# Kernel tuning notes

Hardware: AMD Instinct MI355X
Metric: run time of the kernel (lower is better)

Reference implementation:

```python
import jax, jax.numpy as jnp
import numpy as np

T_DAYS, IN_DIM, H = 50000, 12, 512
PIN, POUT, OUT_DIM = 27, 3, 2
# physical_forward scale factors applied to the column means
SCALES = np.array([400,1,1,1,1,12,10,10,1,1,1,1,1,10,1,1,1,5,1,1,4,1,1,180,1,1,10], np.float32)
# last-layer bias of parnet chosen so constrained params land near published PRELES defaults
BIAS27 = np.array([1.03,0.45,0.118,3.0,0.748,1.1,0.05,1.85,-0.18,0.035,-0.2007,0.5,-0.364,
                   0.0324,0.874,0.07,0.8473,0.12,1.2,0.33,1.0,0.0,0.0,1.1,0.0,0.0,2.0], np.float32)

def _elu(v):
    return jnp.where(v > 0, v, jnp.expm1(v))

def _constrain(p):
    # faithful jax port of parameter_constraint (clamp/relu/sigmoid per column)
    sig = jax.nn.sigmoid
    cols = [jnp.clip(p[:,0],0,2), jax.nn.relu(p[:,1]), jax.nn.relu(p[:,2]), p[:,3],
            jnp.clip(p[:,4],0,2.5), jnp.clip(p[:,5],0.01,3), jnp.clip(p[:,6],-0.2,2.1),
            jnp.clip(p[:,7],0.23,3.0), jnp.clip(p[:,8],-1,0), jnp.clip(p[:,9],0,0.7),
            sig(p[:,10]), p[:,11], p[:,12], jnp.clip(p[:,13],0,1.0), jnp.clip(p[:,14],0,1.2),
            jnp.clip(p[:,15],0,2.5), sig(p[:,16]), jnp.clip(p[:,17],0,1), p[:,18],
            jnp.clip(p[:,19],0,1/0.75), jax.nn.relu(p[:,20]), jax.nn.relu(p[:,21]), p[:,22],
            jax.nn.relu(p[:,23]), jax.nn.relu(p[:,24]), jax.nn.relu(p[:,25]), jax.nn.relu(p[:,26])]
    return jnp.stack(cols, axis=1)

def _preles(pm, cin):
    # PRELES daily LUE model (etmodel=0, LOGFLAG=0, t0=-999 so fPheno=1), run as one lax.scan
    (soildepth, ThetaFC, ThetaPWP, tauDrainage, beta, tau, S0, Smax, kappa, gamma,
     soilthres, bCO2, xCO2, ETbeta, ETkappa, ETchi, ETsoilthres, ETnu, MeltCoef,
     I0, CWmax, SnowThreshold, T0, SWinit, CWinit, SOGinit, Sinit) = [pm[i] for i in range(27)]
    fcap = ThetaFC * soildepth

    def step(carry, day):
        S, theta, snow, canw = carry
        precip, tair, par, vpd, fapar, co2 = day[0], day[1], day[2], day[3], day[4], day[6]
        # temperature acclimation state and fS
        S = S + (tair - S) / tau
        fS = jnp.minimum(jnp.maximum(S - S0, 0.0) / Smax, 1.0)
        # GPP modifiers
        thetavol = theta / soildepth
        REW = (thetavol - ThetaPWP) / (ThetaFC - ThetaPWP)
        fD = jnp.minimum(jnp.exp(kappa * vpd), 1.0)
        fW = jnp.where(REW < soilthres, jnp.where(REW > 0.01, REW / soilthres, 0.0), 1.0)
        fL = 1.0 / (gamma * par + 1.0)
        fE = jnp.minimum(fD, fW)
        gpp380 = beta * par * fapar * fS * fL * fE
        gpp = gpp380 * (1.0 + bCO2 * jnp.log(co2 / 380.0))
        # interception + canopy water store
        intercepted = jnp.where(tair > SnowThreshold, precip * I0 * fapar / 0.75, 0.0)
        rain = precip - intercepted
        cap = CWmax * fapar
        over = intercepted + canw > cap
        small_cw = CWmax <= 1e-8
        tf = jnp.where(small_cw, rain + intercepted,
                       jnp.where(over, rain + intercepted + canw - cap, rain))
        canw = jnp.where(small_cw, canw, jnp.where(over, cap, canw + intercepted))
        # snow pack (degree-day melt)
        newsnow = jnp.where(tair < SnowThreshold, tf, 0.0)
        tf = tf - newsnow
        melt = jnp.where(tair >= T0, MeltCoef * (tair - T0), 0.0)
        melt = jnp.minimum(melt, snow + newsnow)
        snow = snow + newsnow - melt
        # evapotranspiration, etmodel = 0
        fWet = jnp.where(REW < ETsoilthres, jnp.where(REW > 0.01, REW / ETsoilthres, 0.0), 1.0)
        fWet = jnp.where(canw > 1e-8, 1.0, fWet)
        fCO2et = 1.0 + xCO2 * jnp.log(co2 / 380.0)
        transp = vpd * ETbeta * gpp380 / jnp.power(vpd, ETkappa) * jnp.power(jnp.maximum(fW, 1e-12), ETnu) * fCO2et
        evap = ETchi * (1.0 - fapar) * fWet * par
        et = transp + evap
        # soil water balance: evaporate wet canopy then snow, rest from soil
        canw2 = jnp.maximum(canw - et, 0.0)
        rem = jnp.maximum(et - canw, 0.0)
        snow2 = jnp.maximum(snow - rem, 0.0)
        etsoil = jnp.maximum(rem - snow, 0.0)
        st0 = jnp.maximum(theta + tf + melt - etsoil, 1e-4)
        drain = jnp.where(tauDrainage > 0, jnp.maximum(st0 - fcap, 0.0) / tauDrainage, 0.0)
        theta = st0 - drain
        return (S, theta, snow2, canw2), (gpp, et, theta)

    init = (Sinit, SWinit, SOGinit, CWinit)
    _, (GPP, ET, SWout) = jax.lax.scan(step, init, cin)
    return GPP, ET, SWout

def setup_inputs():
    key = jax.random.key(0)
    ks = jax.random.split(key, 12)
    x = jax.random.normal(ks[0], (T_DAYS, IN_DIM), jnp.float32)
    u = jax.random.uniform(ks[1], (T_DAYS, 7), jnp.float32)
    tn = jax.random.normal(ks[2], (T_DAYS,), jnp.float32)
    doy = (jnp.arange(T_DAYS) % 365 + 1).astype(jnp.float32)
    seas = jnp.sin(2 * jnp.pi * (doy - 120) / 365.0)
    precip = jnp.where(u[:, 0] > 0.7, u[:, 0] * 20.0, 0.0)        # mm/day
    tair = 5.0 + 12.0 * seas + 3.0 * tn                            # degC
    par = jnp.maximum(10.0 + 8.0 * seas + 3.0 * jax.random.normal(ks[3], (T_DAYS,), jnp.float32), 0.1)
    vpd = 0.1 + 2.0 * u[:, 3]                                      # kPa, kept > 0.1
    fapar = 0.3 + 0.5 * u[:, 4]
    co2 = 380.0 + 40.0 * u[:, 6]                                   # ppm
    cin = jnp.stack([precip, tair, par, vpd, fapar, doy, co2], axis=1)
    def lin(k, fi, fo, scale, bias=None):
        w = jax.random.normal(k, (fi, fo), jnp.float32) * scale
        b = jnp.zeros((fo,), jnp.float32) if bias is None else jnp.asarray(bias)
        return w, b
    pW0, pb0 = lin(ks[4], IN_DIM, H, 1.0 / np.sqrt(IN_DIM))
    pW1, pb1 = lin(ks[5], H, H, 1.0 / np.sqrt(H))
    pW2, pb2 = lin(ks[6], H, PIN, 0.01, BIAS27)
    rW0, rb0 = lin(ks[7], POUT, H, 1.0 / np.sqrt(POUT))
    rW1, rb1 = lin(ks[8], H, H, 1.0 / np.sqrt(H))
    rW2, rb2 = lin(ks[9], H, OUT_DIM, 1.0 / np.sqrt(H))
    sw = jnp.array([150.0, 50.0], jnp.float32)
    return dict(x=x, cin=cin, sw=sw, tp=1,
                pW0=pW0, pb0=pb0, pW1=pW1, pb1=pb1, pW2=pW2, pb2=pb2,
                rW0=rW0, rb0=rb0, rW1=rW1, rb1=rb1, rW2=rW2, rb2=rb2)

def reference(x, cin, sw, tp, pW0, pb0, pW1, pb1, pW2, pb2, rW0, rb0, rW1, rb1, rW2, rb2):
    # parnet: Linear -> ELU -> Linear -> Linear (single ELU due to add_module name reuse)
    h = _elu(x @ pW0 + pb0)
    h = h @ pW1 + pb1
    praw = h @ pW2 + pb2                      # [T, 27]
    p = _constrain(praw)
    pm = p.mean(axis=0) * jnp.asarray(SCALES)  # per-parameter mean, physical scaling
    GPP, ET, SW = _preles(pm, cin)
    ppreds = jnp.stack([GPP, ET, (SW - sw[0]) / sw[1]], axis=1)  # tp is not None path
    # resnet: Linear -> ELU -> Linear -> Linear
    g = _elu(ppreds @ rW0 + rb0)
    g = g @ rW1 + rb1
    y_hat = g @ rW2 + rb2
    return y_hat, ppreds
```

## Files before the change

kernel.cpp:

```cpp
#include <hip/hip_runtime.h>
#include <hip/hip_bf16.h>

#define T_DAYS   50000
#define HDIM     512
#define NP       27
#define NROWBLK  196

#define NCHUNK   1024
#define CHUNK_L  49
#define WARM     512
#define ITERS    (WARM + CHUNK_L)
#define GRP      8
#define NG       72
#define DPAD     50944
#define DBLK     199

static_assert(NG*GRP >= ITERS, "scan must cover all iterations");
static_assert((NG & 1) == 0, "NG must be even for the ping-pong");
static_assert(1023*CHUNK_L + (NG+1)*GRP - 1 < DPAD, "prefetch stays in padded records");

#define OFF_PJ    0
#define OFF_PR0   20480
#define OFF_RW12  22528
#define OFF_B12   23552
#define OFF_RB12  23579
#define OFF_PART  23584
#define OFF_PM    28880
#define OFF_DA    29184
#define OFF_DB    (OFF_DA + DPAD*4)
#define OFF_DC    (OFF_DB + DPAD*4)
#define OFF_PPT   (OFF_DC + DPAD)
#define WS_FAST_FLOATS (OFF_PPT + CHUNK_L*NCHUNK*3)
#define WS_FAST_BYTES  ((size_t)WS_FAST_FLOATS * 4)

typedef float f32x4 __attribute__((ext_vector_type(4)));

__constant__ float c_SCALES[NP] = {400,1,1,1,1,12,10,10,1,1,1,1,1,10,1,1,1,5,1,1,4,1,1,180,1,1,10};

__device__ __forceinline__ float sane(float v, float lo, float hi) {
  v = (v == v) ? v : 0.f;
  return fminf(fmaxf(v, lo), hi);
}

__device__ __forceinline__ void ldg4(f32x4& d, const f32x4* p) {
  asm volatile("global_load_dwordx4 %0, %1, off" : "=v"(d) : "v"(p));
}
__device__ __forceinline__ void ldg1(float& d, const float* p) {
  asm volatile("global_load_dword %0, %1, off" : "=v"(d) : "v"(p));
}
__device__ __forceinline__ void wait_vm0() {
  asm volatile("s_waitcnt vmcnt(0)" ::: "memory");
  __builtin_amdgcn_sched_barrier(0);
}

__global__ void k_prep(const float* pW0, const float* pb0, const float* pW1,
                       const float* pb1, const float* pW2, const float* pb2,
                       const float* rW0, const float* rb0, const float* rW1,
                       const float* rb1, const float* rW2, const float* rb2,
                       float* ws) {
  __shared__ __align__(16) float col[HDIM];
  const int bid = blockIdx.x, tid = threadIdx.x;
  if (bid < NP) {
    for (int k = tid; k < HDIM; k += 256) col[k] = pW2[k*NP + bid];
    __syncthreads();
    const float4* c4 = (const float4*)col;
    for (int i = tid; i < HDIM; i += 256) {
      const float4* wrow = (const float4*)(pW1 + i*HDIM);
      float acc = 0.f;
      #pragma unroll 4
      for (int k = 0; k < HDIM/4; ++k) {
        float4 w = wrow[k], cv = c4[k];
        acc += w.x*cv.x + w.y*cv.y + w.z*cv.z + w.w*cv.w;
      }
      ws[OFF_PJ + i*40 + 12 + bid] = acc;
    }
    if (tid == 0) {
      float acc = 0.f;
      for (int k = 0; k < HDIM; ++k) acc += pb1[k] * col[k];
      ws[OFF_B12 + bid] = acc + pb2[bid];
    }
  } else if (bid < NP + 2) {
    const int j2 = bid - NP;
    for (int k = tid; k < HDIM; k += 256) col[k] = rW2[k*2 + j2];
    __syncthreads();
    const float4* c4 = (const float4*)col;
    for (int i = tid; i < HDIM; i += 256) {
      const float4* wrow = (const float4*)(rW1 + i*HDIM);
      float acc = 0.f;
      #pragma unroll 4
      for (int k = 0; k < HDIM/4; ++k) {
        float4 w = wrow[k], cv = c4[k];
        acc += w.x*cv.x + w.y*cv.y + w.z*cv.z + w.w*cv.w;
      }
      ws[OFF_RW12 + i*2 + j2] = acc;
    }
    if (tid == 0) {
      float acc = 0.f;
      for (int k = 0; k < HDIM; ++k) acc += rb1[k] * col[k];
      ws[OFF_RB12 + j2] = acc + rb2[j2];
    }
  } else {
    for (int j = tid; j < HDIM; j += 256) {
      for (int k = 0; k < 12; ++k) ws[OFF_PJ + j*40 + k] = pW0[k*HDIM + j];
      ws[OFF_PJ + j*40 + 39] = pb0[j];
      float4 v;
      v.x = rW0[0*HDIM + j]; v.y = rW0[1*HDIM + j];
      v.z = rW0[2*HDIM + j]; v.w = rb0[j];
      ((float4*)(ws + OFF_PR0))[j] = v;
    }
  }
}

__global__ void __launch_bounds__(256) k_parnet(const float* x, float* ws) {
  __shared__ float4 spj[256*10];
  const int t = blockIdx.x*256 + threadIdx.x;

  float xr[12];
  if (t < T_DAYS) {
    const float4* xp = (const float4*)(x + t*12);
    float4 x0 = xp[0], x1 = xp[1], x2 = xp[2];
    xr[0]=x0.x; xr[1]=x0.y; xr[2]=x0.z; xr[3]=x0.w;
    xr[4]=x1.x; xr[5]=x1.y; xr[6]=x1.z; xr[7]=x1.w;
    xr[8]=x2.x; xr[9]=x2.y; xr[10]=x2.z; xr[11]=x2.w;
  } else {
    #pragma unroll
    for (int k = 0; k < 12; ++k) xr[k] = 0.f;
  }

  float acc[NP];
  #pragma unroll
  for (int c = 0; c < NP; ++c) acc[c] = ws[OFF_B12 + c];

  for (int half = 0; half < 2; ++half) {
    __syncthreads();
    const float4* src = ((const float4*)(ws + OFF_PJ)) + half*2560;
    for (int idx = threadIdx.x; idx < 2560; idx += 256) spj[idx] = src[idx];
    __syncthreads();
    for (int j = 0; j < 256; ++j) {
      const float4* row = &spj[j*10];
      float4 a = row[0], b = row[1], cc = row[2];
      float wf[28];
      #pragma unroll
      for (int q = 0; q < 7; ++q) {
        float4 v = row[3 + q];
        wf[4*q] = v.x; wf[4*q+1] = v.y; wf[4*q+2] = v.z; wf[4*q+3] = v.w;
      }
      float h = a.x*xr[0] + a.y*xr[1] + a.z*xr[2] + a.w*xr[3]
              + b.x*xr[4] + b.y*xr[5] + b.z*xr[6] + b.w*xr[7]
              + cc.x*xr[8] + cc.y*xr[9] + cc.z*xr[10] + cc.w*xr[11]
              + wf[27];
      h = h > 0.f ? h : (__expf(h) - 1.f);
      #pragma unroll
      for (int c = 0; c < NP; ++c) acc[c] += h * wf[c];
    }
  }

  auto clip = [] (float v, float lo, float hi) { return fminf(fmaxf(v, lo), hi); };
  acc[0]  = clip(acc[0], 0.f, 2.f);
  acc[1]  = fmaxf(acc[1], 0.f);
  acc[2]  = fmaxf(acc[2], 0.f);
  acc[4]  = clip(acc[4], 0.f, 2.5f);
  acc[5]  = clip(acc[5], 0.01f, 3.f);
  acc[6]  = clip(acc[6], -0.2f, 2.1f);
  acc[7]  = clip(acc[7], 0.23f, 3.0f);
  acc[8]  = clip(acc[8], -1.f, 0.f);
  acc[9]  = clip(acc[9], 0.f, 0.7f);
  acc[10] = 1.f/(1.f + __expf(-acc[10]));
  acc[13] = clip(acc[13], 0.f, 1.0f);
  acc[14] = clip(acc[14], 0.f, 1.2f);
  acc[15] = clip(acc[15], 0.f, 2.5f);
  acc[16] = 1.f/(1.f + __expf(-acc[16]));
  acc[17] = clip(acc[17], 0.f, 1.f);
  acc[19] = clip(acc[19], 0.f, (float)(1.0/0.75));
  acc[20] = fmaxf(acc[20], 0.f);
  acc[21] = fmaxf(acc[21], 0.f);
  acc[23] = fmaxf(acc[23], 0.f);
  acc[24] = fmaxf(acc[24], 0.f);
  acc[25] = fmaxf(acc[25], 0.f);
  acc[26] = fmaxf(acc[26], 0.f);
  if (t >= T_DAYS) {
    #pragma unroll
    for (int c = 0; c < NP; ++c) acc[c] = 0.f;
  }

  #pragma unroll
  for (int c = 0; c < NP; ++c) {
    float v = acc[c];
    #pragma unroll
    for (int off = 32; off >= 1; off >>= 1) v += __shfl_down(v, off, 64);
    acc[c] = v;
  }
  __shared__ float red[4][NP];
  const int wv = threadIdx.x >> 6, ln = threadIdx.x & 63;
  if (ln == 0) {
    #pragma unroll
    for (int c = 0; c < NP; ++c) red[wv][c] = acc[c];
  }
  __syncthreads();
  if (threadIdx.x < NP) {
    float s = red[0][threadIdx.x] + red[1][threadIdx.x] + red[2][threadIdx.x] + red[3][threadIdx.x];
    ws[OFF_PART + blockIdx.x*NP + threadIdx.x] = s;
  }
}

__global__ void k_finalize(float* ws) {
  const int c = threadIdx.x;
  if (c < NP) {
    float s = 0.f;
    for (int b = 0; b < NROWBLK; ++b) s += ws[OFF_PART + b*NP + c];
    ws[OFF_PM + c] = sane(s * (1.f/(float)T_DAYS) * c_SCALES[c], -1e6f, 1e6f);
  }
}

__global__ void __launch_bounds__(256) k_days(const float* ws_in, const float* cin, float* ws) {
  const int tp = blockIdx.x*256 + threadIdx.x;
  if (tp >= DPAD) return;
  const float* pm = ws_in + OFF_PM;
  const float beta = pm[4], kappa = pm[8], gamma = pm[9], bCO2 = pm[11], xCO2 = pm[12];
  const float ETbeta = pm[13], ETkappa = pm[14], ETchi = pm[15], MeltCoef = pm[18];
  const float I0 = pm[19], CWmax = pm[20], SnowThr = pm[21], T0 = pm[22];

  int t = tp - WARM;
  t = t < 0 ? 0 : (t >= T_DAYS ? T_DAYS - 1 : t);
  const float precip = sane(cin[t*7+0], 0.f, 1e4f);
  const float tair   = sane(cin[t*7+1], -150.f, 150.f);
  const float par    = sane(cin[t*7+2], 0.f, 1e4f);
  const float vpd    = sane(cin[t*7+3], 1e-3f, 1e3f);
  const float fapar  = sane(cin[t*7+4], 0.f, 1.f);
  const float co2    = sane(cin[t*7+6], 1.f, 1e5f);

  const float logc = __logf(co2 * (1.f/380.f));
  const float fD   = fminf(__expf(kappa*vpd), 1.f);
  const float G    = beta * par * fapar * (1.f/(gamma*par + 1.f));
  const float Cc   = 1.f + bCO2*logc;
  const float Bq   = ETbeta * __powf(vpd, 1.f - ETkappa) * (1.f + xCO2*logc);
  const float E    = ETchi * (1.f - fapar) * par;
  const float icpt = (tair > SnowThr) ? precip*I0*fapar*(1.f/0.75f) : 0.f;
  const float rain = precip - icpt;
  const float cap  = CWmax * fapar;
  const float mpot = (tair >= T0) ? MeltCoef*(tair - T0) : 0.f;

  ((float4*)(ws + OFF_DA))[tp] = make_float4(fD, G*Cc, Bq*G, E);
  ((float4*)(ws + OFF_DB))[tp] = make_float4(rain, cap, icpt, mpot);
  ws[OFF_DC + tp] = tair;
}

__global__ void __launch_bounds__(64, 1) k_scan_fast(float* ws, const float* sw) {
  const int lane = threadIdx.x;
  const int c = blockIdx.x*64 + lane;
  const float* pm = ws + OFF_PM;
  const float soildepth = pm[0], ThetaFC = pm[1], ThetaPWP = pm[2];
  const float tauD = pm[3], tau = pm[5], S0 = pm[6], Smax = pm[7];
  const float soilthres = pm[10], ETsoilthres = pm[16], ETnu = pm[17];
  const float SnowThr = pm[21];
  const float SWinit = pm[23], CWinit = pm[24], SOGinit = pm[25], Sinit = pm[26];
  const float CWmax = pm[20];

  float dFC = ThetaFC - ThetaPWP; if (!(fabsf(dFC) > 1e-12f)) dFC = 1e-12f;
  float sd  = soildepth;          if (!(fabsf(sd)  > 1e-12f)) sd  = 1e-12f;

  const float invtau = 1.f/fmaxf(tau, 1e-6f), invSmax = 1.f/fmaxf(Smax, 1e-12f);
  const float rc1 = 1.f/(sd*dFC);
  const float rc0 = -ThetaPWP/dFC;
  const float inv_st = 1.f/fmaxf(soilthres, 1e-30f);
  const float inv_est = 1.f/fmaxf(ETsoilthres, 1e-30f);
  const float fcap = ThetaFC*soildepth;
  const float invtauD = (tauD > 0.f) ? 1.f/tauD : 0.f;
  const bool small_cw = (CWmax <= 1e-8f);
  const float sw0 = sane(sw[0], -1e6f, 1e6f);
  const float sw1v = sw[1];
  const float invsw1 = 1.f/((fabsf(sw1v) > 1e-12f) ? sw1v : 1e-12f);

  float S = Sinit, theta = SWinit, snow = SOGinit, canw = CWinit;
  const int i_lo = (c*CHUNK_L < WARM) ? (WARM - c*CHUNK_L) : 0;

  const f32x4* gA = ((const f32x4*)(ws + OFF_DA)) + c*CHUNK_L;
  const f32x4* gB = ((const f32x4*)(ws + OFF_DB)) + c*CHUNK_L;
  const float* gC = (ws + OFF_DC) + c*CHUNK_L;
  float* ppt = ws + OFF_PPT;

  auto step = [&](const f32x4 dA, const f32x4 dB, const float tairv, const int i,
                  float& o0, float& o1, float& o2) {
    if (i < i_lo) return;
    const float fD = dA.x, GC = dA.y, BG = dA.z, E = dA.w;
    const float rain = dB.x, cap = dB.y, icpt = dB.z, mpot = dB.w;

    S += (tairv - S)*invtau;
    S = fminf(fmaxf(S, -1e4f), 1e4f);
    const float fS = fminf(fmaxf(S - S0, 0.f)*invSmax, 1.f);

    const float REW = theta*rc1 + rc0;
    float fW   = (REW >= soilthres)   ? 1.f : ((REW > 0.01f) ? REW*inv_st  : 0.f);
    float fWet = (REW >= ETsoilthres) ? 1.f : ((REW > 0.01f) ? REW*inv_est : 0.f);

    const float precip = rain + icpt;
    const bool over = (icpt + canw > cap);
    const float tf  = small_cw ? precip : (over ? precip + canw - cap : rain);
    const float cw  = small_cw ? canw   : (over ? cap : canw + icpt);
    if (cw > 1e-8f) fWet = 1.f;

    const bool cold = (tairv < SnowThr);
    const float newsnow = cold ? tf : 0.f;
    const float tf2     = cold ? 0.f : tf;
    const float sn = snow + newsnow;
    const float snow_mid = fmaxf(sn - mpot, 0.f);
    const float melt = sn - snow_mid;

    const float sfe = fS * fminf(fD, fW);
    float pw = 1.f;
    if (fW < 1.f) pw = __powf(fmaxf(fW, 1e-12f), ETnu);
    const float transp = BG*sfe*pw;
    const float evap = E*fWet;
    const float et = transp + evap;

    canw = fminf(fmaxf(cw - et, 0.f), 1e4f);
    const float rem = fmaxf(et - cw, 0.f);
    snow = fminf(fmaxf(snow_mid - rem, 0.f), 1e6f);
    const float etsoil = fmaxf(rem - snow_mid, 0.f);
    const float st0 = fmaxf(theta + tf2 + melt - etsoil, 1e-4f);
    const float dr = fmaxf(st0 - fcap, 0.f)*invtauD;
    theta = fminf(fmaxf(st0 - dr, 1e-4f), 1e6f);

    o0 = sane(GC*sfe, -1e6f, 1e6f);
    o1 = sane(et, -1e6f, 1e6f);
    o2 = sane((theta - sw0)*invsw1, -1e6f, 1e6f);
  };

  f32x4 A0[GRP], B0[GRP]; float C0[GRP];
  f32x4 A1[GRP], B1[GRP]; float C1[GRP];
  float poA[GRP*3], poB[GRP*3];

#define ISSUE(GG, A, B, C) do { \
  _Pragma("unroll") for (int k = 0; k < GRP; ++k) { \
    const int ii = (GG)*GRP + k; \
    ldg4(A[k], gA + ii); ldg4(B[k], gB + ii); ldg1(C[k], gC + ii); \
  } __builtin_amdgcn_sched_barrier(0); } while (0)

#define COMPUTE(GG, A, B, C, PO) do { \
  _Pragma("unroll") for (int k = 0; k < GRP; ++k) \
    step(A[k], B[k], C[k], (GG)*GRP + k, PO[k*3], PO[k*3+1], PO[k*3+2]); \
  __builtin_amdgcn_sched_barrier(0); } while (0)

#define FLUSH(GF, PO) do { \
  _Pragma("unroll") for (int k = 0; k < GRP; ++k) { \
    const int io = (GF)*GRP + k - WARM; \
    if (io >= 0 && io < CHUNK_L) { \
      float* pp = ppt + (io*NCHUNK + c)*3; \
      pp[0] = PO[k*3]; pp[1] = PO[k*3+1]; pp[2] = PO[k*3+2]; \
    } } } while (0)

  ISSUE(0, A0, B0, C0);
  for (int g = 0; g < NG; g += 2) {
    wait_vm0();
    ISSUE(g + 1, A1, B1, C1);
    if (g > 0) FLUSH(g - 1, poB);
    COMPUTE(g, A0, B0, C0, poA);

    wait_vm0();
    ISSUE(g + 2, A0, B0, C0);
    FLUSH(g, poA);
    COMPUTE(g + 1, A1, B1, C1, poB);
  }
  FLUSH(NG - 1, poB);

#undef ISSUE
#undef COMPUTE
#undef FLUSH
}

__global__ void __launch_bounds__(256) k_resnet_fast(const float* ws, float* out) {
  __shared__ float4 spr[HDIM];
  __shared__ float2 srw[HDIM];
  for (int idx = threadIdx.x; idx < HDIM; idx += 256) {
    spr[idx] = ((const float4*)(ws + OFF_PR0))[idx];
    srw[idx] = ((const float2*)(ws + OFF_RW12))[idx];
  }
  __syncthreads();
  const int t = blockIdx.x*256 + threadIdx.x;
  if (t >= T_DAYS) return;
  const int c = t / CHUNK_L, i = t - c*CHUNK_L;
  const int r = (i*NCHUNK + c)*3;
  const float p0 = ws[OFF_PPT + r + 0];
  const float p1 = ws[OFF_PPT + r + 1];
  const float p2 = ws[OFF_PPT + r + 2];
  float y0 = ws[OFF_RB12], y1 = ws[OFF_RB12 + 1];
  for (int j = 0; j < HDIM; ++j) {
    const float4 a = spr[j];
    float g = p0*a.x + p1*a.y + p2*a.z + a.w;
    g = g > 0.f ? g : (__expf(g) - 1.f);
    const float2 r2 = srw[j];
    y0 += g*r2.x; y1 += g*r2.y;
  }
  out[t*2 + 0] = sane(y0, -1e6f, 1e6f);
  out[t*2 + 1] = sane(y1, -1e6f, 1e6f);
  out[2*T_DAYS + t*3 + 0] = p0;
  out[2*T_DAYS + t*3 + 1] = p1;
  out[2*T_DAYS + t*3 + 2] = p2;
}

struct DayR { float fD, G, Cc, Bq, E, rain, cap, icpt, mpot, tair; };

__device__ __forceinline__ DayR mkday(const float* cin, int t,
    float beta, float kappa, float gamma, float bCO2, float xCO2, float ETbeta,
    float ETkappa, float ETchi, float MeltCoef, float I0, float CWmax,
    float SnowThr, float T0) {
  int tt = t < 0 ? 0 : (t >= T_DAYS ? T_DAYS - 1 : t);
  const float precip = sane(cin[tt*7+0], 0.f, 1e4f);
  const float tair   = sane(cin[tt*7+1], -150.f, 150.f);
  const float par    = sane(cin[tt*7+2], 0.f, 1e4f);
  const float vpd    = sane(cin[tt*7+3], 1e-3f, 1e3f);
  const float fapar  = sane(cin[tt*7+4], 0.f, 1.f);
  const float co2    = sane(cin[tt*7+6], 1.f, 1e5f);
  const float logc = __logf(co2 * (1.f/380.f));
  DayR d;
  d.fD   = fminf(__expf(kappa*vpd), 1.f);
  d.G    = beta * par * fapar * (1.f/(gamma*par + 1.f));
  d.Cc   = 1.f + bCO2*logc;
  d.Bq   = ETbeta * __powf(vpd, 1.f - ETkappa) * (1.f + xCO2*logc);
  d.E    = ETchi * (1.f - fapar) * par;
  d.icpt = (tair > SnowThr) ? precip*I0*fapar*(1.f/0.75f) : 0.f;
  d.rain = precip - d.icpt;
  d.cap  = CWmax * fapar;
  d.mpot = (tair >= T0) ? MeltCoef*(tair - T0) : 0.f;
  d.tair = tair;
  return d;
}

__global__ void __launch_bounds__(64) k_scan_slow(const float* ws, const float* cin,
                                                 const float* sw, float* out) {
  const int c = blockIdx.x*64 + threadIdx.x;
  const float* pm = ws + OFF_PM;
  const float soildepth = pm[0], ThetaFC = pm[1], ThetaPWP = pm[2];
  const float tauD = pm[3], beta = pm[4], tau = pm[5], S0 = pm[6], Smax = pm[7];
  const float kappa = pm[8], gamma = pm[9], soilthres = pm[10], bCO2 = pm[11];
  const float xCO2 = pm[12], ETbeta = pm[13], ETkappa = pm[14], ETchi = pm[15];
  const float ETsoilthres = pm[16], ETnu = pm[17], MeltCoef = pm[18], I0 = pm[19];
  const float CWmax = pm[20], SnowThr = pm[21], T0 = pm[22];
  const float SWinit = pm[23], CWinit = pm[24], SOGinit = pm[25], Sinit = pm[26];

  float dFC = ThetaFC - ThetaPWP; if (!(fabsf(dFC) > 1e-12f)) dFC = 1e-12f;
  float sd  = soildepth;          if (!(fabsf(sd)  > 1e-12f)) sd  = 1e-12f;

  const float invtau = 1.f/fmaxf(tau, 1e-6f), invSmax = 1.f/fmaxf(Smax, 1e-12f);
  const float rc1 = 1.f/(sd*dFC);
  const float rc0 = -ThetaPWP/dFC;
  const float inv_st = 1.f/fmaxf(soilthres, 1e-30f);
  const float inv_est = 1.f/fmaxf(ETsoilthres, 1e-30f);
  const float fcap = ThetaFC*soildepth;
  const float invtauD = (tauD > 0.f) ? 1.f/tauD : 0.f;
  const bool small_cw = (CWmax <= 1e-8f);
  const float sw0 = sane(sw[0], -1e6f, 1e6f);
  const float sw1v = sw[1];
  const float invsw1 = 1.f/((fabsf(sw1v) > 1e-12f) ? sw1v : 1e-12f);

  float S = Sinit, theta = SWinit, snow = SOGinit, canw = CWinit;
  const int s  = c*CHUNK_L - WARM;
  const int e0 = c*CHUNK_L;

  DayR dA = mkday(cin, s,   beta,kappa,gamma,bCO2,xCO2,ETbeta,ETkappa,ETchi,MeltCoef,I0,CWmax,SnowThr,T0);
  DayR dB = mkday(cin, s+1, beta,kappa,gamma,bCO2,xCO2,ETbeta,ETkappa,ETchi,MeltCoef,I0,CWmax,SnowThr,T0);

  for (int i = 0; i < ITERS; ++i) {
    const DayR d = dA;
    dA = dB;
    dB = mkday(cin, s + i + 2, beta,kappa,gamma,bCO2,xCO2,ETbeta,ETkappa,ETchi,MeltCoef,I0,CWmax,SnowThr,T0);

    const int t = s + i;
    if (t >= 0 && t < T_DAYS) {
      S += (d.tair - S)*invtau;
      S = fminf(fmaxf(S, -1e4f), 1e4f);
      const float fS = fminf(fmaxf(S - S0, 0.f)*invSmax, 1.f);

      const float REW = theta*rc1 + rc0;
      float fW   = (REW >= soilthres)   ? 1.f : ((REW > 0.01f) ? REW*inv_st  : 0.f);
      float fWet = (REW >= ETsoilthres) ? 1.f : ((REW > 0.01f) ? REW*inv_est : 0.f);

      const float precip = d.rain + d.icpt;
      const bool over = (d.icpt + canw > d.cap);
      const float tf  = small_cw ? precip : (over ? precip + canw - d.cap : d.rain);
      const float cw  = small_cw ? canw   : (over ? d.cap : canw + d.icpt);
      if (cw > 1e-8f) fWet = 1.f;

      const bool cold = (d.tair < SnowThr);
      const float newsnow = cold ? tf : 0.f;
      const float tf2     = cold ? 0.f : tf;
      const float sn = snow + newsnow;
      const float snow_mid = fmaxf(sn - d.mpot, 0.f);
      const float melt = sn - snow_mid;

      const float fE = fminf(d.fD, fW);
      const float gpp380 = d.G*fS*fE;
      float pw = 1.f;
      if (fW < 1.f) pw = __powf(fmaxf(fW, 1e-12f), ETnu);
      const float transp = d.Bq*gpp380*pw;
      const float evap = d.E*fWet;
      const float et = transp + evap;

      canw = fminf(fmaxf(cw - et, 0.f), 1e4f);
      const float rem = fmaxf(et - cw, 0.f);
      snow = fminf(fmaxf(snow_mid - rem, 0.f), 1e6f);
      const float etsoil = fmaxf(rem - snow_mid, 0.f);
      const float st0 = fmaxf(theta + tf2 + melt - etsoil, 1e-4f);
      const float dr = fmaxf(st0 - fcap, 0.f)*invtauD;
      theta = fminf(fmaxf(st0 - dr, 1e-4f), 1e6f);

      if (t >= e0) {
        out[2*T_DAYS + t*3 + 0] = sane(gpp380*d.Cc, -1e6f, 1e6f);
        out[2*T_DAYS + t*3 + 1] = sane(et, -1e6f, 1e6f);
        out[2*T_DAYS + t*3 + 2] = sane((theta - sw0)*invsw1, -1e6f, 1e6f);
      }
    }
  }
}

__global__ void __launch_bounds__(256) k_resnet_slow(const float* ws, float* out) {
  const int t = blockIdx.x*256 + threadIdx.x;
  if (t >= T_DAYS) return;
  const float p0 = out[2*T_DAYS + t*3 + 0];
  const float p1 = out[2*T_DAYS + t*3 + 1];
  const float p2 = out[2*T_DAYS + t*3 + 2];
  const float4* pr = (const float4*)(ws + OFF_PR0);
  const float2* rw = (const float2*)(ws + OFF_RW12);
  float y0 = ws[OFF_RB12], y1 = ws[OFF_RB12 + 1];
  for (int j = 0; j < HDIM; ++j) {
    const float4 a = pr[j];
    float g = p0*a.x + p1*a.y + p2*a.z + a.w;
    g = g > 0.f ? g : (__expf(g) - 1.f);
    const float2 r = rw[j];
    y0 += g*r.x; y1 += g*r.y;
  }
  out[t*2 + 0] = sane(y0, -1e6f, 1e6f);
  out[t*2 + 1] = sane(y1, -1e6f, 1e6f);
}

extern "C" void kernel_launch(void* const* d_in, const int* in_sizes, int n_in,
                              void* d_out, int out_size, void* d_ws, size_t ws_size,
                              hipStream_t stream) {
  const float* x   = (const float*)d_in[0];
  const float* cin = (const float*)d_in[1];
  const float* sw  = (const float*)d_in[2];
  const float *pW0 = (const float*)d_in[4],  *pb0 = (const float*)d_in[5];
  const float *pW1 = (const float*)d_in[6],  *pb1 = (const float*)d_in[7];
  const float *pW2 = (const float*)d_in[8],  *pb2 = (const float*)d_in[9];
  const float *rW0 = (const float*)d_in[10], *rb0 = (const float*)d_in[11];
  const float *rW1 = (const float*)d_in[12], *rb1 = (const float*)d_in[13];
  const float *rW2 = (const float*)d_in[14], *rb2 = (const float*)d_in[15];
  float* ws  = (float*)d_ws;
  float* out = (float*)d_out;

  k_prep<<<dim3(NP+3), dim3(256), 0, stream>>>(pW0,pb0,pW1,pb1,pW2,pb2,rW0,rb0,rW1,rb1,rW2,rb2, ws);
  k_parnet<<<dim3(NROWBLK), dim3(256), 0, stream>>>(x, ws);
  k_finalize<<<dim3(1), dim3(32), 0, stream>>>(ws);

  if (ws_size >= WS_FAST_BYTES) {
    k_days<<<dim3(DBLK), dim3(256), 0, stream>>>(ws, cin, ws);
    k_scan_fast<<<dim3(NCHUNK/64), dim3(64), 0, stream>>>(ws, sw);
    k_resnet_fast<<<dim3(NROWBLK), dim3(256), 0, stream>>>(ws, out);
  } else {
    k_scan_slow<<<dim3(NCHUNK/64), dim3(64), 0, stream>>>(ws, cin, sw, out);
    k_resnet_slow<<<dim3(NROWBLK), dim3(256), 0, stream>>>(ws, out);
  }
}
```

Measured before the change: 358.8 us.

## Interleave two independent scan chunks per thread to hide serial dependency latency

Each thread of the chunked PRELES scan now advances two independent chunks (c and c+512) in lockstep, so the two serial dependency chains can interleave and cover each other's instruction latency. The grid is halved to 8 blocks of 64 threads, and the prefetch group shrinks from 8 to 4 days to keep register pressure bounded, with the group count raised to still cover all iterations. In exchange, the kernel uses fewer wavefronts, needs more registers per thread, and loses the warm-up skip optimisation on the second chunk (ilo passed as 0, which is correct since c1 never needs it).

```diff
diff --git a/kernel.cpp b/kernel.cpp
--- a/kernel.cpp
+++ b/kernel.cpp
@@ -10,8 +10,8 @@
 #define CHUNK_L  49
 #define WARM     512
 #define ITERS    (WARM + CHUNK_L)
-#define GRP      8
-#define NG       72
+#define GRP      4
+#define NG       142
 #define DPAD     50944
 #define DBLK     199
 
@@ -247,7 +247,8 @@
 
 __global__ void __launch_bounds__(64, 1) k_scan_fast(float* ws, const float* sw) {
   const int lane = threadIdx.x;
-  const int c = blockIdx.x*64 + lane;
+  const int c0 = blockIdx.x*64 + lane;
+  const int c1 = c0 + NCHUNK/2;
   const float* pm = ws + OFF_PM;
   const float soildepth = pm[0], ThetaFC = pm[1], ThetaPWP = pm[2];
   const float tauD = pm[3], tau = pm[5], S0 = pm[6], Smax = pm[7];
@@ -271,17 +272,23 @@
   const float sw1v = sw[1];
   const float invsw1 = 1.f/((fabsf(sw1v) > 1e-12f) ? sw1v : 1e-12f);
 
-  float S = Sinit, theta = SWinit, snow = SOGinit, canw = CWinit;
-  const int i_lo = (c*CHUNK_L < WARM) ? (WARM - c*CHUNK_L) : 0;
-
-  const f32x4* gA = ((const f32x4*)(ws + OFF_DA)) + c*CHUNK_L;
-  const f32x4* gB = ((const f32x4*)(ws + OFF_DB)) + c*CHUNK_L;
-  const float* gC = (ws + OFF_DC) + c*CHUNK_L;
+  float Sa = Sinit, tha = SWinit, sna = SOGinit, cwa = CWinit;
+  float Sb = Sinit, thb = SWinit, snb = SOGinit, cwb = CWinit;
+  const int ilo0 = (c0*CHUNK_L < WARM) ? (WARM - c0*CHUNK_L) : 0;
+
+  const f32x4* gA0 = ((const f32x4*)(ws + OFF_DA)) + c0*CHUNK_L;
+  const f32x4* gB0 = ((const f32x4*)(ws + OFF_DB)) + c0*CHUNK_L;
+  const float* gC0 = (ws + OFF_DC) + c0*CHUNK_L;
+  const f32x4* gA1 = ((const f32x4*)(ws + OFF_DA)) + c1*CHUNK_L;
+  const f32x4* gB1 = ((const f32x4*)(ws + OFF_DB)) + c1*CHUNK_L;
+  const float* gC1 = (ws + OFF_DC) + c1*CHUNK_L;
   float* ppt = ws + OFF_PPT;
 
-  auto step = [&](const f32x4 dA, const f32x4 dB, const float tairv, const int i,
+  auto step = [&](const f32x4 dA, const f32x4 dB, const float tairv,
+                  const int i, const int ilo,
+                  float& S, float& theta, float& snow, float& canw,
                   float& o0, float& o1, float& o2) {
-    if (i < i_lo) return;
+    if (i < ilo) return;
     const float fD = dA.x, GC = dA.y, BG = dA.z, E = dA.w;
     const float rain = dB.x, cap = dB.y, icpt = dB.z, mpot = dB.w;
 
@@ -326,40 +333,47 @@
     o2 = sane((theta - sw0)*invsw1, -1e6f, 1e6f);
   };
 
-  f32x4 A0[GRP], B0[GRP]; float C0[GRP];
-  f32x4 A1[GRP], B1[GRP]; float C1[GRP];
-  float poA[GRP*3], poB[GRP*3];
-
-#define ISSUE(GG, A, B, C) do { \
+  f32x4 Aa0[GRP], Ba0[GRP]; float Ca0[GRP];
+  f32x4 Ab0[GRP], Bb0[GRP]; float Cb0[GRP];
+  f32x4 Aa1[GRP], Ba1[GRP]; float Ca1[GRP];
+  f32x4 Ab1[GRP], Bb1[GRP]; float Cb1[GRP];
+  float poA[GRP*6], poB[GRP*6];
+
+#define ISSUE(GG, Aa, Ba, Ca, Ab, Bb, Cb) do { \
   _Pragma("unroll") for (int k = 0; k < GRP; ++k) { \
     const int ii = (GG)*GRP + k; \
-    ldg4(A[k], gA + ii); ldg4(B[k], gB + ii); ldg1(C[k], gC + ii); \
+    ldg4(Aa[k], gA0 + ii); ldg4(Ba[k], gB0 + ii); ldg1(Ca[k], gC0 + ii); \
+    ldg4(Ab[k], gA1 + ii); ldg4(Bb[k], gB1 + ii); ldg1(Cb[k], gC1 + ii); \
   } __builtin_amdgcn_sched_barrier(0); } while (0)
 
-#define COMPUTE(GG, A, B, C, PO) do { \
-  _Pragma("unroll") for (int k = 0; k < GRP; ++k) \
-    step(A[k], B[k], C[k], (GG)*GRP + k, PO[k*3], PO[k*3+1], PO[k*3+2]); \
-  __builtin_amdgcn_sched_barrier(0); } while (0)
+#define COMPUTE(GG, Aa, Ba, Ca, Ab, Bb, Cb, PO) do { \
+  _Pragma("unroll") for (int k = 0; k < GRP; ++k) { \
+    const int i = (GG)*GRP + k; \
+    step(Aa[k], Ba[k], Ca[k], i, ilo0, Sa, tha, sna, cwa, PO[k*6+0], PO[k*6+1], PO[k*6+2]); \
+    step(Ab[k], Bb[k], Cb[k], i, 0,    Sb, thb, snb, cwb, PO[k*6+3], PO[k*6+4], PO[k*6+5]); \
+  } __builtin_amdgcn_sched_barrier(0); } while (0)
 
 #define FLUSH(GF, PO) do { \
   _Pragma("unroll") for (int k = 0; k < GRP; ++k) { \
     const int io = (GF)*GRP + k - WARM; \
     if (io >= 0 && io < CHUNK_L) { \
-      float* pp = ppt + (io*NCHUNK + c)*3; \
-      pp[0] = PO[k*3]; pp[1] = PO[k*3+1]; pp[2] = PO[k*3+2]; \
+      float* p0 = ppt + (io*NCHUNK + c0)*3; \
+      p0[0] = PO[k*6+0]; p0[1] = PO[k*6+1]; p0[2] = PO[k*6+2]; \
+      float* p1 = ppt + (io*NCHUNK + c1)*3; \
+      p1[0] = PO[k*6+3]; p1[1] = PO[k*6+4]; p1[2] = PO[k*6+5]; \
     } } } while (0)
 
-  ISSUE(0, A0, B0, C0);
+  ISSUE(0, Aa0, Ba0, Ca0, Ab0, Bb0, Cb0);
   for (int g = 0; g < NG; g += 2) {
     wait_vm0();
-    ISSUE(g + 1, A1, B1, C1);
+    ISSUE(g + 1, Aa1, Ba1, Ca1, Ab1, Bb1, Cb1);
     if (g > 0) FLUSH(g - 1, poB);
-    COMPUTE(g, A0, B0, C0, poA);
+    COMPUTE(g, Aa0, Ba0, Ca0, Ab0, Bb0, Cb0, poA);
 
     wait_vm0();
-    ISSUE(g + 2, A0, B0, C0);
+    ISSUE(g + 2, Aa0, Ba0, Ca0, Ab0, Bb0, Cb0);
     FLUSH(g, poA);
-    COMPUTE(g + 1, A1, B1, C1, poB);
+    COMPUTE(g + 1, Aa1, Ba1, Ca1, Ab1, Bb1, Cb1, poB);
   }
   FLUSH(NG - 1, poB);
 
@@ -554,7 +568,7 @@
 
   if (ws_size >= WS_FAST_BYTES) {
     k_days<<<dim3(DBLK), dim3(256), 0, stream>>>(ws, cin, ws);
-    k_scan_fast<<<dim3(NCHUNK/64), dim3(64), 0, stream>>>(ws, sw);
+    k_scan_fast<<<dim3(NCHUNK/128), dim3(64), 0, stream>>>(ws, sw);
     k_resnet_fast<<<dim3(NROWBLK), dim3(256), 0, stream>>>(ws, out);
   } else {
     k_scan_slow<<<dim3(NCHUNK/64), dim3(64), 0, stream>>>(ws, cin, sw, out);
```

Result: slower. 483.9 us (+34.9%).
